# Kernel tuning notes

Hardware: AMD Instinct MI355X
Metric: run time of the kernel (lower is better)

## Reference

```python
import jax, jax.numpy as jnp
import numpy as np

N, F, M, E = 8192, 256, 128, 131072


def setup_inputs() -> dict:
    key = jax.random.key(0)
    k = jax.random.split(key, 6)
    x = jax.random.normal(k[0], (N, F), dtype=jnp.float32)
    edge_index = jax.random.randint(k[1], (2, E), 0, N, dtype=jnp.int64)
    eps = jax.random.normal(k[2], (N, M), dtype=jnp.float32)
    # small init scale so sigmoid(z_i . z_j) isn't saturated
    W_mu = jax.random.normal(k[3], (F, M), dtype=jnp.float32) * 0.05
    b_mu = jnp.zeros((M,), dtype=jnp.float32)
    W_sig = jax.random.normal(k[4], (F, M), dtype=jnp.float32) * 0.05
    b_sig = jnp.zeros((M,), dtype=jnp.float32)
    return {"x": x, "edge_index": edge_index, "eps": eps,
            "W_mu": W_mu, "b_mu": b_mu, "W_sig": W_sig, "b_sig": b_sig}


def reference(x, edge_index, eps, W_mu, b_mu, W_sig, b_sig):
    # Gaussian encoder: Normal(mu, exp(logstd)), Independent over latent dim
    mu = x @ W_mu + b_mu                      # [N, M]
    logstd = x @ W_sig + b_sig                # [N, M]
    sigma = jnp.exp(logstd)
    z = mu + sigma * eps                      # rsample, [N, M]

    # decoder.probability(dot(z_i, z_j)) = sigmoid(logit); vectorized as Z @ Z.T
    logits = z @ z.T                          # [N, N]

    # symmetric adjacency labels from edge_index (either direction counts)
    src, dst = edge_index[0], edge_index[1]
    adj = jnp.zeros((N, N), dtype=jnp.float32)
    adj = adj.at[src, dst].set(1.0)
    adj = adj.at[dst, src].set(1.0)

    # BCE(sigmoid(s), y) summed over unordered pairs i < j (stable logits form)
    per_pair = jax.nn.softplus(logits) - adj * logits  # = -[y log p + (1-y) log(1-p)]
    triu = jnp.triu(jnp.ones((N, N), dtype=bool), k=1)
    bce = jnp.sum(jnp.where(triu, per_pair, 0.0))

    # sum_i KL( N(mu_i, sigma_i) || N(0, I) )
    kl = jnp.sum(0.5 * (sigma * sigma + mu * mu - 1.0) - logstd)

    return bce + 0.001 * kl
```

## Files before the change

### kernel.cpp

```cpp
#include <hip/hip_runtime.h>

#define NN 8192
#define FF 256
#define MM 128
#define HSLOTS 262144
#define NTILES 2080

typedef __attribute__((ext_vector_type(8))) short bf16x8;
typedef __attribute__((ext_vector_type(4))) float f32x4;

#define P_KL    0
#define P_EDGE  (64 * 16)
#define P_SP    (128 * 16)
#define Z_OFF   16384
#define Z_BYTES (NN * MM * 2)
#define HASH_OFF (Z_OFF + Z_BYTES)
#define WT_OFF  (HASH_OFF + HSLOTS * 4)
#define WT_BYTES (MM * FF * 2)

__device__ __forceinline__ float wave_reduce(float v) {
    #pragma unroll
    for (int off = 32; off > 0; off >>= 1) v += __shfl_down(v, off);
    return v;
}
__device__ __forceinline__ unsigned short f2bf(float f) {
    unsigned int u = __float_as_uint(f);
    u += 0x7fffu + ((u >> 16) & 1u);
    return (unsigned short)(u >> 16);
}
__device__ __forceinline__ int4 pack8(float4 a, float4 b) {
    int4 p;
    p.x = (int)f2bf(a.x) | ((int)f2bf(a.y) << 16);
    p.y = (int)f2bf(a.z) | ((int)f2bf(a.w) << 16);
    p.z = (int)f2bf(b.x) | ((int)f2bf(b.y) << 16);
    p.w = (int)f2bf(b.z) | ((int)f2bf(b.w) << 16);
    return p;
}

__global__ __launch_bounds__(256)
void prep_w(const float* __restrict__ Wmu, const float* __restrict__ Wsg,
            unsigned short* __restrict__ WmuT, unsigned short* __restrict__ WsgT,
            float* __restrict__ part, unsigned int* __restrict__ ht) {
    const int t = blockIdx.x * 256 + threadIdx.x;
    const int n = t >> 8, f = t & 255;
    WmuT[t] = f2bf(Wmu[f * MM + n]);
    WsgT[t] = f2bf(Wsg[f * MM + n]);
    if (t < 4096) part[t] = 0.f;
    uint4 z4 = {0u, 0u, 0u, 0u};
    ((uint4*)ht)[t * 2]     = z4;
    ((uint4*)ht)[t * 2 + 1] = z4;
}

#define XP_I4 33
#define XP_S  264

__global__ __launch_bounds__(256)
void encoder_mfma(const float* __restrict__ x, const float* __restrict__ eps,
                  const unsigned short* __restrict__ WmuT,
                  const unsigned short* __restrict__ WsgT,
                  const float* __restrict__ bmu, const float* __restrict__ bsg,
                  unsigned short* __restrict__ zb, float* __restrict__ part) {
    __shared__ int4 ax[16 * XP_I4];
    __shared__ float red[4];
    const int tid = threadIdx.x;
    const int wid = tid >> 6, lane = tid & 63;
    const int l15 = lane & 15, quad = lane >> 4;
    const int row0 = blockIdx.x * 16;

    {
        const int r = tid >> 4, ch = tid & 15;
        const float4* g0 = (const float4*)(x + (size_t)(row0 + r) * FF + ch * 8);
        const float4* g1 = (const float4*)(x + (size_t)(row0 + r) * FF + (ch + 16) * 8);
        ax[r * XP_I4 + ch]      = pack8(g0[0], g0[1]);
        ax[r * XP_I4 + ch + 16] = pack8(g1[0], g1[1]);
    }
    __syncthreads();

    const short* sax = (const short*)ax;
    const int4* wtm = (const int4*)WmuT;
    const int4* wts = (const int4*)WsgT;

    f32x4 zero4 = {0.f, 0.f, 0.f, 0.f};
    f32x4 accm[2], accl[2];
    accm[0] = accm[1] = accl[0] = accl[1] = zero4;

    #pragma unroll
    for (int ks = 0; ks < 8; ++ks) {
        const bf16x8 a = *(const bf16x8*)&sax[l15 * XP_S + ks * 32 + quad * 8];
        #pragma unroll
        for (int j = 0; j < 2; ++j) {
            const int n = wid * 32 + j * 16 + l15;
            const bf16x8 bmf = *(const bf16x8*)&wtm[n * 32 + ks * 4 + quad];
            const bf16x8 bsf = *(const bf16x8*)&wts[n * 32 + ks * 4 + quad];
            accm[j] = __builtin_amdgcn_mfma_f32_16x16x32_bf16(a, bmf, accm[j], 0, 0, 0);
            accl[j] = __builtin_amdgcn_mfma_f32_16x16x32_bf16(a, bsf, accl[j], 0, 0, 0);
        }
    }

    float klp = 0.f;
    #pragma unroll
    for (int j = 0; j < 2; ++j) {
        const int col = wid * 32 + j * 16 + l15;
        const float bm = bmu[col], bs = bsg[col];
        #pragma unroll
        for (int r = 0; r < 4; ++r) {
            const int row = row0 + quad * 4 + r;
            const float mu = accm[j][r] + bm;
            const float ls = accl[j][r] + bs;
            const float sg = __expf(ls);
            const float zz = fmaf(sg, eps[(size_t)row * MM + col], mu);
            zb[(size_t)row * MM + col] = f2bf(zz);
            klp += 0.5f * (sg * sg + mu * mu - 1.f) - ls;
        }
    }

    klp = wave_reduce(klp);
    if (lane == 0) red[wid] = klp;
    __syncthreads();
    if (tid == 0)
        atomicAdd(&part[P_KL + (blockIdx.x & 63) * 16],
                  red[0] + red[1] + red[2] + red[3]);
}

__device__ __forceinline__ float dotpair(unsigned int a, unsigned int b) {
    const float al = __uint_as_float(a << 16);
    const float ah = __uint_as_float(a & 0xffff0000u);
    const float bl = __uint_as_float(b << 16);
    const float bh = __uint_as_float(b & 0xffff0000u);
    return fmaf(al, bl, ah * bh);
}

__global__ __launch_bounds__(256, 3)
void tile_edge_kernel(const unsigned short* __restrict__ zb,
                      const int* __restrict__ ei, int E, int NE,
                      unsigned int* __restrict__ ht,
                      float* __restrict__ part) {
    __shared__ int4 la[128 * 8];
    __shared__ int4 lb[128 * 8];

    const int tid = threadIdx.x;
    const int bid = blockIdx.x;

    int bi = (int)((129.0f - sqrtf(16641.0f - 8.0f * (float)bid)) * 0.5f);
    bi = min(max(bi, 0), 63);
    while ((bi * (129 - bi)) / 2 > bid) --bi;
    while (((bi + 1) * (128 - bi)) / 2 <= bid) ++bi;
    const int bj = bi + (bid - (bi * (129 - bi)) / 2);

    const int wid = tid >> 6, lane = tid & 63;
    const int wm = wid >> 1, wn = wid & 1;
    const int l15 = lane & 15, quad = lane >> 4;
    const int xk = l15 & 7;

    const int4* ga = (const int4*)(zb + (size_t)bi * 128 * MM);
    const int4* gb = (const int4*)(zb + (size_t)bj * 128 * MM);

    f32x4 zero4 = {0.f, 0.f, 0.f, 0.f};
    f32x4 acc[4][4];
    #pragma unroll
    for (int i = 0; i < 4; ++i)
        #pragma unroll
        for (int j = 0; j < 4; ++j) acc[i][j] = zero4;

    const short* sa = (const short*)la;
    const short* sb = (const short*)lb;

    #pragma unroll
    for (int kc = 0; kc < 2; ++kc) {
        if (kc) __syncthreads();
        #pragma unroll
        for (int i = 0; i < 4; ++i) {
            const int c = tid + i * 256;
            const int row = c >> 3, ch = c & 7;
            const int sl = ch ^ (row & 7);
            la[row * 8 + sl] = ga[row * 16 + kc * 8 + ch];
            lb[row * 8 + sl] = gb[row * 16 + kc * 8 + ch];
        }
        __syncthreads();
        #pragma unroll
        for (int ks = 0; ks < 2; ++ks) {
            const int kq = ks * 4 + quad;
            bf16x8 af[4], bfr[4];
            #pragma unroll
            for (int t2 = 0; t2 < 4; ++t2) {
                const int ar = wm * 64 + t2 * 16 + l15;
                af[t2]  = *(const bf16x8*)&sa[ar * 64 + ((kq ^ xk) * 8)];
                const int br = wn * 64 + t2 * 16 + l15;
                bfr[t2] = *(const bf16x8*)&sb[br * 64 + ((kq ^ xk) * 8)];
            }
            #pragma unroll
            for (int i = 0; i < 4; ++i)
                #pragma unroll
                for (int j = 0; j < 4; ++j)
                    acc[i][j] = __builtin_amdgcn_mfma_f32_16x16x32_bf16(
                        af[i], bfr[j], acc[i][j], 0, 0, 0);
        }
    }

    float tsum = 0.f;
    if (bi != bj) {
        #pragma unroll
        for (int i = 0; i < 4; ++i)
            #pragma unroll
            for (int j = 0; j < 4; ++j)
                #pragma unroll
                for (int r = 0; r < 4; ++r) {
                    const float v = acc[i][j][r];
                    const float e = __expf(-fabsf(v));
                    tsum += fmaxf(v, 0.f) + e * fmaf(e, -0.5f, 1.f);
                }
    } else {
        const int rbase = wm * 64 + quad * 4;
        const int cbase = wn * 64 + l15;
        #pragma unroll
        for (int i = 0; i < 4; ++i)
            #pragma unroll
            for (int j = 0; j < 4; ++j)
                #pragma unroll
                for (int r = 0; r < 4; ++r)
                    if (cbase + j * 16 > rbase + i * 16 + r) {
                        const float v = acc[i][j][r];
                        const float e = __expf(-fabsf(v));
                        tsum += fmaxf(v, 0.f) + e * fmaf(e, -0.5f, 1.f);
                    }
    }

    tsum = wave_reduce(tsum);
    if (lane == 0)
        atomicAdd(&part[P_SP + ((bi * 64 + bj + wid * 16) & 63) * 16], tsum);

    if (bid < NE) {
        const int e = bid * 256 + tid;
        float contrib = 0.f;
        if (e < E) {
            const int i = ei[e];
            const int j = ei[E + e];
            if (i != j) {
                const int a = min(i, j), b = max(i, j);
                const unsigned int key = (unsigned int)a * NN + b;
                unsigned int slot = (key * 2654435761u) & (HSLOTS - 1);
                bool first = false;
                for (;;) {
                    const unsigned int old = atomicCAS(&ht[slot], 0u, key);
                    if (old == 0u) { first = true; break; }
                    if (old == key) break;
                    slot = (slot + 1) & (HSLOTS - 1);
                }
                if (first) {
                    const uint4* za = (const uint4*)(zb + (size_t)a * MM);
                    const uint4* zc = (const uint4*)(zb + (size_t)b * MM);
                    float s = 0.f;
                    #pragma unroll
                    for (int q = 0; q < MM / 8; ++q) {
                        const uint4 ua = za[q], ub = zc[q];
                        s += dotpair(ua.x, ub.x) + dotpair(ua.y, ub.y)
                           + dotpair(ua.z, ub.z) + dotpair(ua.w, ub.w);
                    }
                    contrib = s;
                }
            }
        }
        contrib = wave_reduce(contrib);
        if ((tid & 63) == 0)
            atomicAdd(&part[P_EDGE + (bid & 63) * 16], contrib);
    }
}

__global__ void combine_kernel(const float* __restrict__ part,
                               float* __restrict__ out) {
    const int t = threadIdx.x;
    float v = part[P_SP + t * 16] - part[P_EDGE + t * 16]
            + 0.001f * part[P_KL + t * 16];
    v = wave_reduce(v);
    if (t == 0) out[0] = v;
}

extern "C" void kernel_launch(void* const* d_in, const int* in_sizes, int n_in,
                              void* d_out, int out_size, void* d_ws, size_t ws_size,
                              hipStream_t stream) {
    const float* x   = (const float*)d_in[0];
    const int* ei    = (const int*)d_in[1];
    const float* eps = (const float*)d_in[2];
    const float* Wmu = (const float*)d_in[3];
    const float* bmu = (const float*)d_in[4];
    const float* Wsg = (const float*)d_in[5];
    const float* bsg = (const float*)d_in[6];
    float* out = (float*)d_out;
    char* ws = (char*)d_ws;

    float* part = (float*)ws;
    unsigned short* zb = (unsigned short*)(ws + Z_OFF);
    unsigned int* ht = (unsigned int*)(ws + HASH_OFF);
    unsigned short* WmuT = (unsigned short*)(ws + WT_OFF);
    unsigned short* WsgT = (unsigned short*)(ws + WT_OFF + WT_BYTES);
    const int E = in_sizes[1] / 2;
    const int NE = (E + 255) / 256;

    prep_w<<<128, 256, 0, stream>>>(Wmu, Wsg, WmuT, WsgT, part, ht);
    encoder_mfma<<<NN / 16, 256, 0, stream>>>(x, eps, WmuT, WsgT, bmu, bsg, zb, part);
    tile_edge_kernel<<<NTILES, 256, 0, stream>>>(zb, ei, E, NE, ht, part);
    combine_kernel<<<1, 64, 0, stream>>>(part, out);
}
```

Measured before the change: 113.9 us.

## Use direct global-to-LDS loads, remap tiles, raise occupancy, fuse final combine

Tile staging now uses global_load_lds so 16-byte chunks go straight into shared memory without passing through registers, with the XOR swizzle moved to the source address. Tile indices are permuted across blocks, occupancy is raised from 3 to 4 blocks per SM, and the separate combine kernel is replaced by a last-block-done counter inside the tile kernel. This aims to cut register pressure, launch overhead and load latency, but relies on the counter slot being zeroed in prep and on correct memory ordering for the last-block reduction.

```diff
diff --git a/kernel.cpp b/kernel.cpp
--- a/kernel.cpp
+++ b/kernel.cpp
@@ -12,6 +12,7 @@
 #define P_KL    0
 #define P_EDGE  (64 * 16)
 #define P_SP    (128 * 16)
+#define P_CNT   3072
 #define Z_OFF   16384
 #define Z_BYTES (NN * MM * 2)
 #define HASH_OFF (Z_OFF + Z_BYTES)
@@ -35,6 +36,11 @@
     p.z = (int)f2bf(b.x) | ((int)f2bf(b.y) << 16);
     p.w = (int)f2bf(b.z) | ((int)f2bf(b.w) << 16);
     return p;
+}
+__device__ __forceinline__ void gload16(const void* gsrc, void* ldst) {
+    __builtin_amdgcn_global_load_lds(
+        (const __attribute__((address_space(1))) void*)gsrc,
+        (__attribute__((address_space(3))) void*)ldst, 16, 0, 0);
 }
 
 __global__ __launch_bounds__(256)
@@ -130,22 +136,24 @@
     return fmaf(al, bl, ah * bh);
 }
 
-__global__ __launch_bounds__(256, 3)
+__global__ __launch_bounds__(256, 4)
 void tile_edge_kernel(const unsigned short* __restrict__ zb,
                       const int* __restrict__ ei, int E, int NE,
                       unsigned int* __restrict__ ht,
-                      float* __restrict__ part) {
+                      float* __restrict__ part, float* __restrict__ out) {
     __shared__ int4 la[128 * 8];
     __shared__ int4 lb[128 * 8];
+    __shared__ int lastflag;
 
     const int tid = threadIdx.x;
     const int bid = blockIdx.x;
-
-    int bi = (int)((129.0f - sqrtf(16641.0f - 8.0f * (float)bid)) * 0.5f);
+    const int tl = (bid & 7) * (NTILES / 8) + (bid >> 3);
+
+    int bi = (int)((129.0f - sqrtf(16641.0f - 8.0f * (float)tl)) * 0.5f);
     bi = min(max(bi, 0), 63);
-    while ((bi * (129 - bi)) / 2 > bid) --bi;
-    while (((bi + 1) * (128 - bi)) / 2 <= bid) ++bi;
-    const int bj = bi + (bid - (bi * (129 - bi)) / 2);
+    while ((bi * (129 - bi)) / 2 > tl) --bi;
+    while (((bi + 1) * (128 - bi)) / 2 <= tl) ++bi;
+    const int bj = bi + (tl - (bi * (129 - bi)) / 2);
 
     const int wid = tid >> 6, lane = tid & 63;
     const int wm = wid >> 1, wn = wid & 1;
@@ -171,10 +179,10 @@
         #pragma unroll
         for (int i = 0; i < 4; ++i) {
             const int c = tid + i * 256;
-            const int row = c >> 3, ch = c & 7;
-            const int sl = ch ^ (row & 7);
-            la[row * 8 + sl] = ga[row * 16 + kc * 8 + ch];
-            lb[row * 8 + sl] = gb[row * 16 + kc * 8 + ch];
+            const int row = c >> 3, sl = c & 7;
+            const int ch = sl ^ (row & 7);
+            gload16(&ga[row * 16 + kc * 8 + ch], &la[c]);
+            gload16(&gb[row * 16 + kc * 8 + ch], &lb[c]);
         }
         __syncthreads();
         #pragma unroll
@@ -264,15 +272,28 @@
         if ((tid & 63) == 0)
             atomicAdd(&part[P_EDGE + (bid & 63) * 16], contrib);
     }
-}
-
-__global__ void combine_kernel(const float* __restrict__ part,
-                               float* __restrict__ out) {
-    const int t = threadIdx.x;
-    float v = part[P_SP + t * 16] - part[P_EDGE + t * 16]
-            + 0.001f * part[P_KL + t * 16];
-    v = wave_reduce(v);
-    if (t == 0) out[0] = v;
+
+    __syncthreads();
+    if (tid == 0) {
+        unsigned int* cnt = reinterpret_cast<unsigned int*>(part) + P_CNT;
+        const unsigned int old = __hip_atomic_fetch_add(
+            cnt, 1u, __ATOMIC_RELAXED, __HIP_MEMORY_SCOPE_AGENT);
+        lastflag = (old == (unsigned int)gridDim.x - 1u) ? 1 : 0;
+    }
+    __syncthreads();
+    if (lastflag && tid < 64) {
+        float* psp = &part[P_SP + tid * 16];
+        float* ped = &part[P_EDGE + tid * 16];
+        float* pkl = &part[P_KL + tid * 16];
+        float v = __hip_atomic_fetch_add(psp, 0.f, __ATOMIC_RELAXED,
+                                         __HIP_MEMORY_SCOPE_AGENT)
+                - __hip_atomic_fetch_add(ped, 0.f, __ATOMIC_RELAXED,
+                                         __HIP_MEMORY_SCOPE_AGENT)
+                + 0.001f * __hip_atomic_fetch_add(pkl, 0.f, __ATOMIC_RELAXED,
+                                                  __HIP_MEMORY_SCOPE_AGENT);
+        v = wave_reduce(v);
+        if (tid == 0) out[0] = v;
+    }
 }
 
 extern "C" void kernel_launch(void* const* d_in, const int* in_sizes, int n_in,
@@ -298,6 +319,5 @@
 
     prep_w<<<128, 256, 0, stream>>>(Wmu, Wsg, WmuT, WsgT, part, ht);
     encoder_mfma<<<NN / 16, 256, 0, stream>>>(x, eps, WmuT, WsgT, bmu, bsg, zb, part);
-    tile_edge_kernel<<<NTILES, 256, 0, stream>>>(zb, ei, E, NE, ht, part);
-    combine_kernel<<<1, 64, 0, stream>>>(part, out);
-}
+    tile_edge_kernel<<<NTILES, 256, 0, stream>>>(zb, ei, E, NE, ht, part, out);
+}
```

Result: slower. 122.0 us (+7.1%).
